# Performance work log

Measured on AMD Instinct MI355X. Metric: run time of the kernel, lower is better.

Reference implementation:

```python
import jax, jax.numpy as jnp
import numpy as np

DIM = 768
HEADS = 12
HEAD_DIM = DIM // HEADS
B, N = 8, 512
LN_EPS = 1e-5


def setup_inputs() -> dict:
    key = jax.random.key(0)
    ks = jax.random.split(key, 6)
    x = jax.random.normal(ks[0], (B, N, DIM), dtype=jnp.float32)
    qkv_w = jax.random.normal(ks[1], (3 * DIM, DIM), dtype=jnp.float32) * (DIM ** -0.5)
    ln_w = jnp.ones((HEADS, N, N), dtype=jnp.float32)
    ln_b = jnp.zeros((HEADS, N, N), dtype=jnp.float32)
    proj_w = jax.random.normal(ks[2], (DIM, DIM), dtype=jnp.float32) * (DIM ** -0.5)
    proj_b = jnp.zeros((DIM,), dtype=jnp.float32)
    return {"x": x, "qkv_w": qkv_w, "ln_w": ln_w, "ln_b": ln_b,
            "proj_w": proj_w, "proj_b": proj_b}


def _grassmannian(t):
    # project each head vector onto the unit sphere (L2 normalize over head_dim)
    nrm = jnp.linalg.norm(t, axis=-1, keepdims=True)
    return t / nrm


def reference(x, qkv_w, ln_w, ln_b, proj_w, proj_b):
    b, n, c = x.shape
    qkv = (x @ qkv_w.T).reshape(b, n, 3, HEADS, HEAD_DIM)
    qkv = jnp.transpose(qkv, (2, 0, 3, 1, 4))  # (3, B, H, N, d)
    q, k, v = qkv[0], qkv[1], qkv[2]
    q = _grassmannian(q)
    k = _grassmannian(k)
    # ||outer(q_n, k_m)||_2^2 over head_dim == sum_d q_d^2 k_d^2 = (q^2) @ (k^2)^T
    attn = jnp.einsum('bhnd,bhmd->bhnm', q * q, k * k)  # (B, H, N, N)
    # LayerNorm over normalized_shape=(H, N, N), i.e. per batch element
    mean = jnp.mean(attn, axis=(1, 2, 3), keepdims=True)
    var = jnp.var(attn, axis=(1, 2, 3), keepdims=True)
    attn = (attn - mean) * jax.lax.rsqrt(var + LN_EPS) * ln_w + ln_b
    out = jnp.einsum('bhnm,bhmd->bhnd', attn, v)  # (B, H, N, d)
    out = jnp.transpose(out, (0, 2, 1, 3)).reshape(b, n, c)
    out = out @ proj_w.T + proj_b
    return out, attn
```

## Files before the change

kernel.cpp:

```cpp
#include <hip/hip_runtime.h>

typedef __attribute__((ext_vector_type(8))) short bf16x8;
typedef __attribute__((ext_vector_type(4))) float f32x4;

#define HEADS 12
#define NN 512
#define BB 8
#define DIM 768
#define LDK 72
#define LDK32 40
#define OUT0_ELEMS ((size_t)BB*NN*DIM)

__device__ __forceinline__ ushort f2bf(float f) {
  union { float f; uint u; } v; v.f = f;
  uint r = v.u + 0x7fffu + ((v.u >> 16) & 1u);
  return (ushort)(r >> 16);
}

__global__ __launch_bounds__(256) void cvt_kernel(const float* __restrict__ in,
                                                  ushort* __restrict__ out, int n8) {
  int i = blockIdx.x * 256 + threadIdx.x;
  if (i >= n8) return;
  float4 a = ((const float4*)in)[i*2], b = ((const float4*)in)[i*2+1];
  uint4 o;
  o.x = f2bf(a.x) | ((uint)f2bf(a.y) << 16);
  o.y = f2bf(a.z) | ((uint)f2bf(a.w) << 16);
  o.z = f2bf(b.x) | ((uint)f2bf(b.y) << 16);
  o.w = f2bf(b.z) | ((uint)f2bf(b.w) << 16);
  ((uint4*)out)[i] = o;
}

__global__ __launch_bounds__(256) void qkv_gemm(
    const float* __restrict__ x, const ushort* __restrict__ wb,
    ushort* __restrict__ q2b, ushort* __restrict__ k2b, ushort* __restrict__ vt)
{
  __shared__ ushort As[128 * LDK];
  __shared__ ushort Bs[128 * LDK];
  const int t = threadIdx.x, l = t & 63, w = t >> 6;
  const int bx = blockIdx.x, by = blockIdx.y;
  const int rowbase = by * 128, colbase = bx * 128;
  const int wr = w >> 1, wc = w & 1, lr = l & 15, lg = l >> 4;
  f32x4 acc[4][4] = {};

  for (int kc = 0; kc < DIM; kc += 64) {
    #pragma unroll
    for (int i = 0; i < 4; ++i) {
      int c = t + 256 * i;
      int r = c >> 3, k16 = c & 7;
      const float* src = x + (size_t)(rowbase + r) * DIM + kc + k16 * 8;
      float4 v0 = *(const float4*)src, v1 = *(const float4*)(src + 4);
      uint4 pk;
      pk.x = f2bf(v0.x) | ((uint)f2bf(v0.y) << 16);
      pk.y = f2bf(v0.z) | ((uint)f2bf(v0.w) << 16);
      pk.z = f2bf(v1.x) | ((uint)f2bf(v1.y) << 16);
      pk.w = f2bf(v1.z) | ((uint)f2bf(v1.w) << 16);
      *(uint4*)(As + r * LDK + k16 * 8) = pk;
      *(uint4*)(Bs + r * LDK + k16 * 8) =
          *(const uint4*)(wb + (size_t)(colbase + r) * DIM + kc + k16 * 8);
    }
    __syncthreads();
    #pragma unroll
    for (int ks = 0; ks < 2; ++ks) {
      bf16x8 af[4], bg[4];
      #pragma unroll
      for (int i = 0; i < 4; ++i)
        af[i] = *(const bf16x8*)(As + (wr*64 + i*16 + lr) * LDK + ks*32 + lg*8);
      #pragma unroll
      for (int j = 0; j < 4; ++j)
        bg[j] = *(const bf16x8*)(Bs + (wc*64 + j*16 + lr) * LDK + ks*32 + lg*8);
      #pragma unroll
      for (int i = 0; i < 4; ++i)
        #pragma unroll
        for (int j = 0; j < 4; ++j)
          acc[i][j] = __builtin_amdgcn_mfma_f32_16x16x32_bf16(af[i], bg[j], acc[i][j], 0, 0, 0);
    }
    __syncthreads();
  }

  const int gcol = colbase + wc * 64;
  const int sel = gcol / DIM;
  const int h = (gcol % DIM) / 64;
  if (sel < 2) {
    ushort* dst = (sel == 0) ? q2b : k2b;
    #pragma unroll
    for (int i = 0; i < 4; ++i) {
      #pragma unroll
      for (int r = 0; r < 4; ++r) {
        float vj[4]; float s = 0.f;
        #pragma unroll
        for (int j = 0; j < 4; ++j) { vj[j] = acc[i][j][r]; s += vj[j] * vj[j]; }
        #pragma unroll
        for (int off = 1; off < 16; off <<= 1) s += __shfl_xor(s, off);
        float inv = 1.0f / s;
        int row = rowbase + wr*64 + i*16 + lg*4 + r;
        int b = row >> 9, n = row & 511;
        ushort* o = dst + (((size_t)(b * HEADS + h) * NN + n) << 6);
        #pragma unroll
        for (int j = 0; j < 4; ++j) o[j*16 + lr] = f2bf(vj[j] * vj[j] * inv);
      }
    }
  } else {
    #pragma unroll
    for (int i = 0; i < 4; ++i) {
      int row0 = rowbase + wr*64 + i*16 + lg*4;
      int b = row0 >> 9, n0 = row0 & 511;
      #pragma unroll
      for (int j = 0; j < 4; ++j) {
        int d = j*16 + lr;
        ushort4 pk;
        pk.x = f2bf(acc[i][j][0]); pk.y = f2bf(acc[i][j][1]);
        pk.z = f2bf(acc[i][j][2]); pk.w = f2bf(acc[i][j][3]);
        *(ushort4*)(vt + (((size_t)(b * HEADS + h) * 64 + d) << 9) + n0) = pk;
      }
    }
  }
}

__global__ __launch_bounds__(256) void attn_gemm(
    const ushort* __restrict__ q2b, const ushort* __restrict__ k2b,
    float* __restrict__ attn, double* __restrict__ hsum)
{
  __shared__ ushort As[128 * LDK];
  __shared__ ushort Bs[128 * LDK];
  __shared__ float red[8];
  const int t = threadIdx.x, l = t & 63, w = t >> 6;
  const int tile = blockIdx.x, h = blockIdx.y, b = blockIdx.z;
  const int rowbase = (tile >> 2) * 128, colbase = (tile & 3) * 128;
  const size_t bh = (size_t)(b * HEADS + h);
  const ushort* Aq = q2b + (bh << 15) + ((size_t)rowbase << 6);
  const ushort* Bk = k2b + (bh << 15) + ((size_t)colbase << 6);
  #pragma unroll
  for (int i = 0; i < 4; ++i) {
    int c = t + 256 * i;
    int r = c >> 3, k16 = c & 7;
    *(uint4*)(As + r * LDK + k16 * 8) = *(const uint4*)(Aq + ((size_t)r << 6) + k16 * 8);
    *(uint4*)(Bs + r * LDK + k16 * 8) = *(const uint4*)(Bk + ((size_t)r << 6) + k16 * 8);
  }
  __syncthreads();
  const int wr = w >> 1, wc = w & 1, lr = l & 15, lg = l >> 4;
  f32x4 acc[4][4] = {};
  #pragma unroll
  for (int ks = 0; ks < 2; ++ks) {
    bf16x8 af[4], bg[4];
    #pragma unroll
    for (int i = 0; i < 4; ++i)
      af[i] = *(const bf16x8*)(As + (wr*64 + i*16 + lr) * LDK + ks*32 + lg*8);
    #pragma unroll
    for (int j = 0; j < 4; ++j)
      bg[j] = *(const bf16x8*)(Bs + (wc*64 + j*16 + lr) * LDK + ks*32 + lg*8);
    #pragma unroll
    for (int i = 0; i < 4; ++i)
      #pragma unroll
      for (int j = 0; j < 4; ++j)
        acc[i][j] = __builtin_amdgcn_mfma_f32_16x16x32_bf16(af[i], bg[j], acc[i][j], 0, 0, 0);
  }
  float s1 = 0.f, s2 = 0.f;
  float* op = attn + ((bh << 9) + rowbase) * NN + colbase;
  #pragma unroll
  for (int i = 0; i < 4; ++i) {
    #pragma unroll
    for (int r = 0; r < 4; ++r) {
      int rr = wr*64 + i*16 + lg*4 + r;
      #pragma unroll
      for (int j = 0; j < 4; ++j) {
        float val = acc[i][j][r];
        s1 += val; s2 += val * val;
        op[(size_t)rr * NN + wc*64 + j*16 + lr] = val;
      }
    }
  }
  #pragma unroll
  for (int off = 1; off < 64; off <<= 1) { s1 += __shfl_xor(s1, off); s2 += __shfl_xor(s2, off); }
  if (l == 0) { red[w] = s1; red[4 + w] = s2; }
  __syncthreads();
  if (t == 0) {
    double d1 = (double)red[0] + red[1] + red[2] + red[3];
    double d2 = (double)red[4] + red[5] + red[6] + red[7];
    atomicAdd(&hsum[b * 2], d1);
    atomicAdd(&hsum[b * 2 + 1], d2);
  }
}

__global__ __launch_bounds__(256) void norm_pv(
    float* __restrict__ attn, const ushort* __restrict__ vt,
    const float* __restrict__ lnw, const float* __restrict__ lnb,
    const double* __restrict__ hsum, ushort* __restrict__ obh)
{
  __shared__ ushort As[128 * LDK32];
  __shared__ ushort Bs[64 * LDK32];
  const int t = threadIdx.x, l = t & 63, w = t >> 6;
  const int rt = blockIdx.x, h = blockIdx.y, b = blockIdx.z;
  const int rowbase = rt * 128;
  const size_t bh = (size_t)(b * HEADS + h);
  const double cnt = (double)HEADS * NN * NN;
  double mu = hsum[b * 2] / cnt;
  double var = hsum[b * 2 + 1] / cnt - mu * mu;
  const float mean = (float)mu;
  const float istd = (float)(1.0 / sqrt(var + 1e-5));
  float* arow = attn + ((bh << 9) + rowbase) * NN;
  const float* lwr = lnw + ((size_t)h * NN + rowbase) * NN;
  const float* lbr = lnb + ((size_t)h * NN + rowbase) * NN;
  const ushort* V = vt + (bh << 15);
  const int lr = l & 15, lg = l >> 4;
  f32x4 acc[2][4] = {};

  for (int kc = 0; kc < NN; kc += 32) {
    #pragma unroll
    for (int i = 0; i < 4; ++i) {
      int c = t + 256 * i;
      int r = c >> 3, q4 = c & 7;
      size_t g = (size_t)r * NN + kc + q4 * 4;
      float4 av = *(const float4*)(arow + g);
      float4 lw = *(const float4*)(lwr + g);
      float4 lb = *(const float4*)(lbr + g);
      float4 nv;
      nv.x = (av.x - mean) * istd * lw.x + lb.x;
      nv.y = (av.y - mean) * istd * lw.y + lb.y;
      nv.z = (av.z - mean) * istd * lw.z + lb.z;
      nv.w = (av.w - mean) * istd * lw.w + lb.w;
      *(float4*)(arow + g) = nv;
      uint2 pk;
      pk.x = f2bf(nv.x) | ((uint)f2bf(nv.y) << 16);
      pk.y = f2bf(nv.z) | ((uint)f2bf(nv.w) << 16);
      *(uint2*)(As + r * LDK32 + q4 * 4) = pk;
    }
    {
      int r = t >> 2, k16 = t & 3;
      *(uint4*)(Bs + r * LDK32 + k16 * 8) =
          *(const uint4*)(V + ((size_t)r << 9) + kc + k16 * 8);
    }
    __syncthreads();
    bf16x8 af[2], bg[4];
    #pragma unroll
    for (int i = 0; i < 2; ++i)
      af[i] = *(const bf16x8*)(As + (w*32 + i*16 + lr) * LDK32 + lg*8);
    #pragma unroll
    for (int j = 0; j < 4; ++j)
      bg[j] = *(const bf16x8*)(Bs + (j*16 + lr) * LDK32 + lg*8);
    #pragma unroll
    for (int i = 0; i < 2; ++i)
      #pragma unroll
      for (int j = 0; j < 4; ++j)
        acc[i][j] = __builtin_amdgcn_mfma_f32_16x16x32_bf16(af[i], bg[j], acc[i][j], 0, 0, 0);
    __syncthreads();
  }
  #pragma unroll
  for (int i = 0; i < 2; ++i) {
    int gr = b * NN + rowbase + w*32 + i*16 + lg*4;
    #pragma unroll
    for (int j = 0; j < 4; ++j) {
      int gc = h * 64 + j*16 + lr;
      #pragma unroll
      for (int r = 0; r < 4; ++r)
        obh[(size_t)(gr + r) * DIM + gc] = f2bf(acc[i][j][r]);
    }
  }
}

__global__ __launch_bounds__(256) void proj_gemm(
    const ushort* __restrict__ obh, const ushort* __restrict__ pwb,
    const float* __restrict__ pb, float* __restrict__ out)
{
  __shared__ ushort As[128 * LDK];
  __shared__ ushort Bs[128 * LDK];
  const int t = threadIdx.x, l = t & 63, w = t >> 6;
  const int bx = blockIdx.x, by = blockIdx.y;
  const int rowbase = by * 128, colbase = bx * 128;
  const int wr = w >> 1, wc = w & 1, lr = l & 15, lg = l >> 4;
  f32x4 acc[4][4] = {};
  for (int kc = 0; kc < DIM; kc += 64) {
    #pragma unroll
    for (int i = 0; i < 4; ++i) {
      int c = t + 256 * i;
      int r = c >> 3, k16 = c & 7;
      *(uint4*)(As + r * LDK + k16 * 8) =
          *(const uint4*)(obh + (size_t)(rowbase + r) * DIM + kc + k16 * 8);
      *(uint4*)(Bs + r * LDK + k16 * 8) =
          *(const uint4*)(pwb + (size_t)(colbase + r) * DIM + kc + k16 * 8);
    }
    __syncthreads();
    #pragma unroll
    for (int ks = 0; ks < 2; ++ks) {
      bf16x8 af[4], bg[4];
      #pragma unroll
      for (int i = 0; i < 4; ++i)
        af[i] = *(const bf16x8*)(As + (wr*64 + i*16 + lr) * LDK + ks*32 + lg*8);
      #pragma unroll
      for (int j = 0; j < 4; ++j)
        bg[j] = *(const bf16x8*)(Bs + (wc*64 + j*16 + lr) * LDK + ks*32 + lg*8);
      #pragma unroll
      for (int i = 0; i < 4; ++i)
        #pragma unroll
        for (int j = 0; j < 4; ++j)
          acc[i][j] = __builtin_amdgcn_mfma_f32_16x16x32_bf16(af[i], bg[j], acc[i][j], 0, 0, 0);
    }
    __syncthreads();
  }
  #pragma unroll
  for (int i = 0; i < 4; ++i) {
    #pragma unroll
    for (int r = 0; r < 4; ++r) {
      int row = rowbase + wr*64 + i*16 + lg*4 + r;
      #pragma unroll
      for (int j = 0; j < 4; ++j) {
        int col = colbase + wc*64 + j*16 + lr;
        out[(size_t)row * DIM + col] = acc[i][j][r] + pb[col];
      }
    }
  }
}

extern "C" void kernel_launch(void* const* d_in, const int* in_sizes, int n_in,
                              void* d_out, int out_size, void* d_ws, size_t ws_size,
                              hipStream_t stream) {
  const float* x      = (const float*)d_in[0];
  const float* qkv_w  = (const float*)d_in[1];
  const float* ln_w   = (const float*)d_in[2];
  const float* ln_b   = (const float*)d_in[3];
  const float* proj_w = (const float*)d_in[4];
  const float* proj_b = (const float*)d_in[5];
  float* out      = (float*)d_out;
  float* attn_out = out + OUT0_ELEMS;

  char* ws = (char*)d_ws;
  double* hsum = (double*)ws;
  ushort* wb   = (ushort*)(ws + 256);
  ushort* pwb  = wb + (size_t)2304 * 768;
  ushort* q2b  = pwb + (size_t)768 * 768;
  ushort* k2b  = q2b + ((size_t)BB * HEADS * NN << 6);
  ushort* vt   = k2b + ((size_t)BB * HEADS * NN << 6);
  ushort* obh  = vt  + ((size_t)BB * HEADS * NN << 6);

  hipMemsetAsync(hsum, 0, 256, stream);
  cvt_kernel<<<dim3(864), 256, 0, stream>>>(qkv_w, wb, 221184);
  cvt_kernel<<<dim3(288), 256, 0, stream>>>(proj_w, pwb, 73728);
  qkv_gemm  <<<dim3(18, 32),     256, 0, stream>>>(x, wb, q2b, k2b, vt);
  attn_gemm <<<dim3(16, HEADS, BB), 256, 0, stream>>>(q2b, k2b, attn_out, hsum);
  norm_pv   <<<dim3(4, HEADS, BB),  256, 0, stream>>>(attn_out, vt, ln_w, ln_b, hsum, obh);
  proj_gemm <<<dim3(6, 32),      256, 0, stream>>>(obh, pwb, proj_b, out);
}
```

Before: 317.2 us.

## Recompute QK^T in norm kernel instead of storing and rereading attn

The attention GEMM no longer writes raw scores. A stats-only kernel computes the LayerNorm sums from Q and K, and the norm_pv kernel recomputes QK^T per tile, applies the LayerNorm, writes attn once with nontemporal stores and feeds bf16 P through shared memory into the PV MFMA. This removes a full fp32 write and read of the attention tensor at the cost of doing QK^T twice. x is also pre-converted to bf16 by a separate cvt kernel, so qkv_gemm reads bf16 directly.

```diff
diff --git a/kernel.cpp b/kernel.cpp
--- a/kernel.cpp
+++ b/kernel.cpp
@@ -8,7 +8,7 @@
 #define BB 8
 #define DIM 768
 #define LDK 72
-#define LDK32 40
+#define LDV 136
 #define OUT0_ELEMS ((size_t)BB*NN*DIM)
 
 __device__ __forceinline__ ushort f2bf(float f) {
@@ -31,7 +31,7 @@
 }
 
 __global__ __launch_bounds__(256) void qkv_gemm(
-    const float* __restrict__ x, const ushort* __restrict__ wb,
+    const ushort* __restrict__ xb, const ushort* __restrict__ wb,
     ushort* __restrict__ q2b, ushort* __restrict__ k2b, ushort* __restrict__ vt)
 {
   __shared__ ushort As[128 * LDK];
@@ -47,14 +47,8 @@
     for (int i = 0; i < 4; ++i) {
       int c = t + 256 * i;
       int r = c >> 3, k16 = c & 7;
-      const float* src = x + (size_t)(rowbase + r) * DIM + kc + k16 * 8;
-      float4 v0 = *(const float4*)src, v1 = *(const float4*)(src + 4);
-      uint4 pk;
-      pk.x = f2bf(v0.x) | ((uint)f2bf(v0.y) << 16);
-      pk.y = f2bf(v0.z) | ((uint)f2bf(v0.w) << 16);
-      pk.z = f2bf(v1.x) | ((uint)f2bf(v1.y) << 16);
-      pk.w = f2bf(v1.z) | ((uint)f2bf(v1.w) << 16);
-      *(uint4*)(As + r * LDK + k16 * 8) = pk;
+      *(uint4*)(As + r * LDK + k16 * 8) =
+          *(const uint4*)(xb + (size_t)(rowbase + r) * DIM + kc + k16 * 8);
       *(uint4*)(Bs + r * LDK + k16 * 8) =
           *(const uint4*)(wb + (size_t)(colbase + r) * DIM + kc + k16 * 8);
     }
@@ -116,58 +110,55 @@
   }
 }
 
-__global__ __launch_bounds__(256) void attn_gemm(
+__global__ __launch_bounds__(256) void stats_kernel(
     const ushort* __restrict__ q2b, const ushort* __restrict__ k2b,
-    float* __restrict__ attn, double* __restrict__ hsum)
+    double* __restrict__ hsum)
 {
-  __shared__ ushort As[128 * LDK];
-  __shared__ ushort Bs[128 * LDK];
+  __shared__ ushort Qs[256 * LDK];
+  __shared__ ushort Ks[128 * LDK];
   __shared__ float red[8];
   const int t = threadIdx.x, l = t & 63, w = t >> 6;
-  const int tile = blockIdx.x, h = blockIdx.y, b = blockIdx.z;
-  const int rowbase = (tile >> 2) * 128, colbase = (tile & 3) * 128;
+  const int rt = blockIdx.x, h = blockIdx.y, b = blockIdx.z;
   const size_t bh = (size_t)(b * HEADS + h);
-  const ushort* Aq = q2b + (bh << 15) + ((size_t)rowbase << 6);
-  const ushort* Bk = k2b + (bh << 15) + ((size_t)colbase << 6);
-  #pragma unroll
-  for (int i = 0; i < 4; ++i) {
+  const int rowbase = rt * 256;
+  const int lr = l & 15, lg = l >> 4;
+  #pragma unroll
+  for (int i = 0; i < 8; ++i) {
     int c = t + 256 * i;
     int r = c >> 3, k16 = c & 7;
-    *(uint4*)(As + r * LDK + k16 * 8) = *(const uint4*)(Aq + ((size_t)r << 6) + k16 * 8);
-    *(uint4*)(Bs + r * LDK + k16 * 8) = *(const uint4*)(Bk + ((size_t)r << 6) + k16 * 8);
-  }
-  __syncthreads();
-  const int wr = w >> 1, wc = w & 1, lr = l & 15, lg = l >> 4;
-  f32x4 acc[4][4] = {};
-  #pragma unroll
-  for (int ks = 0; ks < 2; ++ks) {
-    bf16x8 af[4], bg[4];
+    *(uint4*)(Qs + r * LDK + k16 * 8) =
+        *(const uint4*)(q2b + (bh << 15) + ((size_t)(rowbase + r) << 6) + k16 * 8);
+  }
+  float s1 = 0.f, s2 = 0.f;
+  for (int ct = 0; ct < 4; ++ct) {
+    #pragma unroll
+    for (int i = 0; i < 4; ++i) {
+      int c = t + 256 * i;
+      int r = c >> 3, k16 = c & 7;
+      *(uint4*)(Ks + r * LDK + k16 * 8) =
+          *(const uint4*)(k2b + (bh << 15) + ((size_t)(ct*128 + r) << 6) + k16 * 8);
+    }
+    __syncthreads();
+    bf16x8 af[4][2];
     #pragma unroll
     for (int i = 0; i < 4; ++i)
-      af[i] = *(const bf16x8*)(As + (wr*64 + i*16 + lr) * LDK + ks*32 + lg*8);
-    #pragma unroll
-    for (int j = 0; j < 4; ++j)
-      bg[j] = *(const bf16x8*)(Bs + (wc*64 + j*16 + lr) * LDK + ks*32 + lg*8);
-    #pragma unroll
-    for (int i = 0; i < 4; ++i)
-      #pragma unroll
-      for (int j = 0; j < 4; ++j)
-        acc[i][j] = __builtin_amdgcn_mfma_f32_16x16x32_bf16(af[i], bg[j], acc[i][j], 0, 0, 0);
-  }
-  float s1 = 0.f, s2 = 0.f;
-  float* op = attn + ((bh << 9) + rowbase) * NN + colbase;
-  #pragma unroll
-  for (int i = 0; i < 4; ++i) {
-    #pragma unroll
-    for (int r = 0; r < 4; ++r) {
-      int rr = wr*64 + i*16 + lg*4 + r;
-      #pragma unroll
-      for (int j = 0; j < 4; ++j) {
-        float val = acc[i][j][r];
-        s1 += val; s2 += val * val;
-        op[(size_t)rr * NN + wc*64 + j*16 + lr] = val;
-      }
-    }
+      #pragma unroll
+      for (int ks = 0; ks < 2; ++ks)
+        af[i][ks] = *(const bf16x8*)(Qs + (w*64 + i*16 + lr) * LDK + ks*32 + lg*8);
+    #pragma unroll
+    for (int j = 0; j < 8; ++j) {
+      bf16x8 b0 = *(const bf16x8*)(Ks + (j*16 + lr) * LDK + lg*8);
+      bf16x8 b1 = *(const bf16x8*)(Ks + (j*16 + lr) * LDK + 32 + lg*8);
+      #pragma unroll
+      for (int i = 0; i < 4; ++i) {
+        f32x4 a = {};
+        a = __builtin_amdgcn_mfma_f32_16x16x32_bf16(af[i][0], b0, a, 0, 0, 0);
+        a = __builtin_amdgcn_mfma_f32_16x16x32_bf16(af[i][1], b1, a, 0, 0, 0);
+        #pragma unroll
+        for (int r = 0; r < 4; ++r) { s1 += a[r]; s2 += a[r]*a[r]; }
+      }
+    }
+    __syncthreads();
   }
   #pragma unroll
   for (int off = 1; off < 64; off <<= 1) { s1 += __shfl_xor(s1, off); s2 += __shfl_xor(s2, off); }
@@ -182,77 +173,97 @@
 }
 
 __global__ __launch_bounds__(256) void norm_pv(
-    float* __restrict__ attn, const ushort* __restrict__ vt,
+    const ushort* __restrict__ q2b, const ushort* __restrict__ k2b,
+    const ushort* __restrict__ vt,
     const float* __restrict__ lnw, const float* __restrict__ lnb,
-    const double* __restrict__ hsum, ushort* __restrict__ obh)
+    const double* __restrict__ hsum,
+    float* __restrict__ attn, ushort* __restrict__ obh)
 {
-  __shared__ ushort As[128 * LDK32];
-  __shared__ ushort Bs[64 * LDK32];
+  __shared__ ushort Qs[64 * LDK];
+  __shared__ ushort Ks[128 * LDK];
+  __shared__ ushort Vs[64 * LDV];
+  __shared__ ushort Ps[64 * LDV];
   const int t = threadIdx.x, l = t & 63, w = t >> 6;
   const int rt = blockIdx.x, h = blockIdx.y, b = blockIdx.z;
-  const int rowbase = rt * 128;
   const size_t bh = (size_t)(b * HEADS + h);
+  const int rowbase = rt * 64;
+  const int lr = l & 15, lg = l >> 4;
   const double cnt = (double)HEADS * NN * NN;
   double mu = hsum[b * 2] / cnt;
   double var = hsum[b * 2 + 1] / cnt - mu * mu;
   const float mean = (float)mu;
   const float istd = (float)(1.0 / sqrt(var + 1e-5));
-  float* arow = attn + ((bh << 9) + rowbase) * NN;
-  const float* lwr = lnw + ((size_t)h * NN + rowbase) * NN;
-  const float* lbr = lnb + ((size_t)h * NN + rowbase) * NN;
-  const ushort* V = vt + (bh << 15);
-  const int lr = l & 15, lg = l >> 4;
-  f32x4 acc[2][4] = {};
-
-  for (int kc = 0; kc < NN; kc += 32) {
-    #pragma unroll
-    for (int i = 0; i < 4; ++i) {
-      int c = t + 256 * i;
-      int r = c >> 3, q4 = c & 7;
-      size_t g = (size_t)r * NN + kc + q4 * 4;
-      float4 av = *(const float4*)(arow + g);
-      float4 lw = *(const float4*)(lwr + g);
-      float4 lb = *(const float4*)(lbr + g);
-      float4 nv;
-      nv.x = (av.x - mean) * istd * lw.x + lb.x;
-      nv.y = (av.y - mean) * istd * lw.y + lb.y;
-      nv.z = (av.z - mean) * istd * lw.z + lb.z;
-      nv.w = (av.w - mean) * istd * lw.w + lb.w;
-      *(float4*)(arow + g) = nv;
-      uint2 pk;
-      pk.x = f2bf(nv.x) | ((uint)f2bf(nv.y) << 16);
-      pk.y = f2bf(nv.z) | ((uint)f2bf(nv.w) << 16);
-      *(uint2*)(As + r * LDK32 + q4 * 4) = pk;
-    }
-    {
-      int r = t >> 2, k16 = t & 3;
-      *(uint4*)(Bs + r * LDK32 + k16 * 8) =
-          *(const uint4*)(V + ((size_t)r << 9) + kc + k16 * 8);
-    }
-    __syncthreads();
-    bf16x8 af[2], bg[4];
-    #pragma unroll
-    for (int i = 0; i < 2; ++i)
-      af[i] = *(const bf16x8*)(As + (w*32 + i*16 + lr) * LDK32 + lg*8);
-    #pragma unroll
-    for (int j = 0; j < 4; ++j)
-      bg[j] = *(const bf16x8*)(Bs + (j*16 + lr) * LDK32 + lg*8);
-    #pragma unroll
-    for (int i = 0; i < 2; ++i)
-      #pragma unroll
-      for (int j = 0; j < 4; ++j)
-        acc[i][j] = __builtin_amdgcn_mfma_f32_16x16x32_bf16(af[i], bg[j], acc[i][j], 0, 0, 0);
-    __syncthreads();
-  }
+
   #pragma unroll
   for (int i = 0; i < 2; ++i) {
-    int gr = b * NN + rowbase + w*32 + i*16 + lg*4;
-    #pragma unroll
-    for (int j = 0; j < 4; ++j) {
-      int gc = h * 64 + j*16 + lr;
-      #pragma unroll
-      for (int r = 0; r < 4; ++r)
-        obh[(size_t)(gr + r) * DIM + gc] = f2bf(acc[i][j][r]);
+    int c = t + 256 * i;
+    int r = c >> 3, k16 = c & 7;
+    *(uint4*)(Qs + r * LDK + k16 * 8) =
+        *(const uint4*)(q2b + (bh << 15) + ((size_t)(rowbase + r) << 6) + k16 * 8);
+  }
+  f32x4 opv[4] = {};
+
+  for (int ct = 0; ct < 4; ++ct) {
+    #pragma unroll
+    for (int i = 0; i < 4; ++i) {
+      int c = t + 256 * i;
+      int r = c >> 3, k16 = c & 7;
+      *(uint4*)(Ks + r * LDK + k16 * 8) =
+          *(const uint4*)(k2b + (bh << 15) + ((size_t)(ct*128 + r) << 6) + k16 * 8);
+    }
+    #pragma unroll
+    for (int i = 0; i < 4; ++i) {
+      int c = t + 256 * i;
+      int r = c >> 4, k16 = c & 15;
+      *(uint4*)(Vs + r * LDV + k16 * 8) =
+          *(const uint4*)(vt + (bh << 15) + ((size_t)r << 9) + ct*128 + k16 * 8);
+    }
+    __syncthreads();
+    #pragma unroll
+    for (int i = 0; i < 4; ++i) {
+      bf16x8 a0 = *(const bf16x8*)(Qs + (i*16 + lr) * LDK + lg*8);
+      bf16x8 a1 = *(const bf16x8*)(Qs + (i*16 + lr) * LDK + 32 + lg*8);
+      #pragma unroll
+      for (int j = 0; j < 2; ++j) {
+        bf16x8 b0 = *(const bf16x8*)(Ks + (w*32 + j*16 + lr) * LDK + lg*8);
+        bf16x8 b1 = *(const bf16x8*)(Ks + (w*32 + j*16 + lr) * LDK + 32 + lg*8);
+        f32x4 a = {};
+        a = __builtin_amdgcn_mfma_f32_16x16x32_bf16(a0, b0, a, 0, 0, 0);
+        a = __builtin_amdgcn_mfma_f32_16x16x32_bf16(a1, b1, a, 0, 0, 0);
+        const int nl = i*16 + lg*4;
+        const int ml = w*32 + j*16 + lr;
+        const int n = rowbase + nl;
+        const int m = ct*128 + ml;
+        const float* lwp = lnw + ((size_t)h * NN + n) * NN + m;
+        const float* lbp = lnb + ((size_t)h * NN + n) * NN + m;
+        float* ap = attn + ((bh << 9) + n) * NN + m;
+        #pragma unroll
+        for (int r = 0; r < 4; ++r) {
+          float v = (a[r] - mean) * istd * lwp[(size_t)r * NN] + lbp[(size_t)r * NN];
+          __builtin_nontemporal_store(v, ap + (size_t)r * NN);
+          Ps[(nl + r) * LDV + ml] = f2bf(v);
+        }
+      }
+    }
+    __syncthreads();
+    #pragma unroll
+    for (int ks = 0; ks < 4; ++ks) {
+      bf16x8 ap = *(const bf16x8*)(Ps + (w*16 + lr) * LDV + ks*32 + lg*8);
+      #pragma unroll
+      for (int j = 0; j < 4; ++j) {
+        bf16x8 bv = *(const bf16x8*)(Vs + (j*16 + lr) * LDV + ks*32 + lg*8);
+        opv[j] = __builtin_amdgcn_mfma_f32_16x16x32_bf16(ap, bv, opv[j], 0, 0, 0);
+      }
+    }
+    __syncthreads();
+  }
+  #pragma unroll
+  for (int j = 0; j < 4; ++j) {
+    int gc = h * 64 + j*16 + lr;
+    #pragma unroll
+    for (int r = 0; r < 4; ++r) {
+      int gr = b * NN + rowbase + w*16 + lg*4 + r;
+      obh[(size_t)gr * DIM + gc] = f2bf(opv[j][r]);
     }
   }
 }
@@ -325,17 +336,20 @@
   char* ws = (char*)d_ws;
   double* hsum = (double*)ws;
   ushort* wb   = (ushort*)(ws + 256);
-  ushort* pwb  = wb + (size_t)2304 * 768;
-  ushort* q2b  = pwb + (size_t)768 * 768;
+  ushort* pwb  = wb  + (size_t)2304 * 768;
+  ushort* xb   = pwb + (size_t)768 * 768;
+  ushort* q2b  = xb  + (size_t)4096 * 768;
   ushort* k2b  = q2b + ((size_t)BB * HEADS * NN << 6);
   ushort* vt   = k2b + ((size_t)BB * HEADS * NN << 6);
   ushort* obh  = vt  + ((size_t)BB * HEADS * NN << 6);
 
-  hipMemsetAsync(hsum, 0, 256, stream);
-  cvt_kernel<<<dim3(864), 256, 0, stream>>>(qkv_w, wb, 221184);
-  cvt_kernel<<<dim3(288), 256, 0, stream>>>(proj_w, pwb, 73728);
-  qkv_gemm  <<<dim3(18, 32),     256, 0, stream>>>(x, wb, q2b, k2b, vt);
-  attn_gemm <<<dim3(16, HEADS, BB), 256, 0, stream>>>(q2b, k2b, attn_out, hsum);
-  norm_pv   <<<dim3(4, HEADS, BB),  256, 0, stream>>>(attn_out, vt, ln_w, ln_b, hsum, obh);
-  proj_gemm <<<dim3(6, 32),      256, 0, stream>>>(obh, pwb, proj_b, out);
-}
+  hipMemsetAsync(hsum, 0, 128, stream);
+  cvt_kernel<<<dim3(864),  256, 0, stream>>>(qkv_w,  wb,  221184);
+  cvt_kernel<<<dim3(288),  256, 0, stream>>>(proj_w, pwb, 73728);
+  cvt_kernel<<<dim3(1536), 256, 0, stream>>>(x,      xb,  393216);
+  qkv_gemm    <<<dim3(18, 32),        256, 0, stream>>>(xb, wb, q2b, k2b, vt);
+  stats_kernel<<<dim3(2, HEADS, BB),  256, 0, stream>>>(q2b, k2b, hsum);
+  norm_pv     <<<dim3(8, HEADS, BB),  256, 0, stream>>>(q2b, k2b, vt, ln_w, ln_b, hsum,
+                                                        attn_out, obh);
+  proj_gemm   <<<dim3(6, 32),         256, 0, stream>>>(obh, pwb, proj_b, out);
+}
```

New measurement: 259.9 us. 18.1% less time.
